# Optimization experiments

Measured on AMD Instinct MI355X. Metric: run time of the kernel, lower is better.

## Reference

```python
import jax, jax.numpy as jnp
import numpy as np

TOKENS = 32768
HIDDEN = 2048
N_EXPERTS = 128
TOP_K = 8
NORM_TOPK_PROB = True


def setup_inputs() -> dict:
    key = jax.random.key(0)
    k1, k2 = jax.random.split(key)
    hidden_states = jax.random.normal(k1, (TOKENS, HIDDEN), dtype=jnp.float32)
    # router weight [num_experts, hidden_dim]; small init like a trained gate
    weight = jax.random.normal(k2, (N_EXPERTS, HIDDEN), dtype=jnp.float32) * 0.02
    return {"hidden_states": hidden_states, "weight": weight}


def reference(hidden_states, weight):
    # flatten tokens (already [T, H])
    x = hidden_states.reshape(-1, HIDDEN)
    # router logits: [T, E]
    logits = jnp.einsum("th,eh->te", x, weight)
    # softmax in float32 (matches dtype=torch.float)
    probs = jax.nn.softmax(logits.astype(jnp.float32), axis=-1)
    # top-k over experts
    top_val, top_idx = jax.lax.top_k(probs, TOP_K)  # [T, K], [T, K]
    if NORM_TOPK_PROB:
        top_val = top_val / jnp.sum(top_val, axis=-1, keepdims=True)
    top_val = top_val.astype(probs.dtype)
    # scatter renormalized weights into dense [T, E] score tensor
    rows = jnp.arange(x.shape[0])[:, None]  # [T, 1]
    scores = jnp.zeros_like(probs).at[rows, top_idx].set(top_val)
    return scores, top_idx
```

## Files before the change

kernel.cpp:

```cpp
#include <hip/hip_runtime.h>
#include <hip/hip_bf16.h>

#define NT   32768
#define NH   2048
#define NE   128
#define TOPK 8
#define BT   32
#define BND    6.0e-4f
#define TWO_B  (2.0f * BND)

#define WS_W_OFF   64
#define WS_REC_U32 262160

typedef __attribute__((ext_vector_type(8))) short bf16x8;
typedef __attribute__((ext_vector_type(4))) float f32x4;
typedef __attribute__((ext_vector_type(4))) unsigned int u32x4;

static __device__ __forceinline__ unsigned short f2bf(float f) {
    __hip_bfloat16 h = __float2bfloat16(f);
    return *reinterpret_cast<unsigned short*>(&h);
}

__global__ __launch_bounds__(256) void prep_w_kernel(
    const float* __restrict__ W, unsigned short* __restrict__ Wt)
{
    int g = blockIdx.x * 256 + threadIdx.x;
    int lane = g & 63;
    int te   = (g >> 6) & 7;
    int s    = (g >> 9) & 1;
    int k32  = g >> 10;
    int row  = te * 16 + (lane & 15);
    int kb   = k32 * 32 + (lane >> 4) * 8;
    const float* src = W + (size_t)row * NH + kb;
    float4 f0 = *(const float4*)src;
    float4 f1 = *(const float4*)(src + 4);
    float f[8] = {f0.x, f0.y, f0.z, f0.w, f1.x, f1.y, f1.z, f1.w};
    bf16x8 o;
    #pragma unroll
    for (int e = 0; e < 8; ++e) {
        unsigned short h = f2bf(f[e]);
        if (s == 0) o[e] = (short)h;
        else {
            float fh = __builtin_bit_cast(float, ((unsigned int)h) << 16);
            o[e] = (short)f2bf(f[e] - fh);
        }
    }
    *(bf16x8*)(Wt + (size_t)g * 8) = o;
}

__global__ __launch_bounds__(256, 2) void router_gemm_kernel(
    const float* __restrict__ X, const unsigned short* __restrict__ Wt,
    float* __restrict__ out, unsigned int* __restrict__ ws)
{
    __shared__ float ps[2][BT * 132];

    const int tid  = threadIdx.x;
    const int lane = tid & 63;
    const int w    = tid >> 6;
    const int l15  = lane & 15, lhi = lane >> 4;
    const int t0   = blockIdx.x * BT;

    f32x4 acc[2][8];
    #pragma unroll
    for (int i = 0; i < 2; ++i)
        #pragma unroll
        for (int te = 0; te < 8; ++te) acc[i][te] = (f32x4){0.f, 0.f, 0.f, 0.f};

    const float* x0 = X + (size_t)(t0 + l15) * NH + w * 512 + lhi * 8;
    const float* x1 = x0 + 16 * NH;
    const unsigned short* wbase = Wt + (size_t)(w * 16) * 8192 + lane * 8;

    bf16x8 b0[8][2], b1[8][2];

    #define LOADB(arr, kk) do {                                                \
        const unsigned short* wb_ = wbase + (size_t)(kk) * 8192;               \
        _Pragma("unroll")                                                      \
        for (int te = 0; te < 8; ++te) {                                       \
            arr[te][0] = *(const bf16x8*)(wb_ + te * 512);                     \
            arr[te][1] = *(const bf16x8*)(wb_ + 4096 + te * 512);              \
        }                                                                      \
    } while (0)

    #define SPLITA(kk, ah, al) do {                                            \
        _Pragma("unroll")                                                      \
        for (int i = 0; i < 2; ++i) {                                          \
            const float* xp = (i ? x1 : x0) + (kk) * 32;                       \
            float4 fa = *(const float4*)xp;                                    \
            float4 fb = *(const float4*)(xp + 4);                              \
            float ff[8] = {fa.x, fa.y, fa.z, fa.w, fb.x, fb.y, fb.z, fb.w};    \
            unsigned int hu[4], lu[4];                                         \
            _Pragma("unroll")                                                  \
            for (int p = 0; p < 4; ++p) {                                      \
                unsigned int u0 = __builtin_bit_cast(unsigned int, ff[2*p]);   \
                unsigned int u1 = __builtin_bit_cast(unsigned int, ff[2*p+1]); \
                unsigned int r0 = u0 + 0x8000u, r1 = u1 + 0x8000u;             \
                hu[p] = (r0 >> 16) | (r1 & 0xFFFF0000u);                       \
                float h0 = __builtin_bit_cast(float, r0 & 0xFFFF0000u);        \
                float h1 = __builtin_bit_cast(float, r1 & 0xFFFF0000u);        \
                float e0 = ff[2*p] - h0, e1 = ff[2*p+1] - h1;                  \
                unsigned int s0 = __builtin_bit_cast(unsigned int, e0) + 0x8000u; \
                unsigned int s1 = __builtin_bit_cast(unsigned int, e1) + 0x8000u; \
                lu[p] = (s0 >> 16) | (s1 & 0xFFFF0000u);                       \
            }                                                                  \
            ah[i] = __builtin_bit_cast(bf16x8, (u32x4){hu[0],hu[1],hu[2],hu[3]}); \
            al[i] = __builtin_bit_cast(bf16x8, (u32x4){lu[0],lu[1],lu[2],lu[3]}); \
        }                                                                      \
    } while (0)

    #define DOMFMA(b, ah, al) do {                                             \
        _Pragma("unroll")                                                      \
        for (int te = 0; te < 8; ++te) {                                       \
            acc[0][te] = __builtin_amdgcn_mfma_f32_16x16x32_bf16(ah[0], b[te][0], acc[0][te], 0, 0, 0); \
            acc[1][te] = __builtin_amdgcn_mfma_f32_16x16x32_bf16(ah[1], b[te][0], acc[1][te], 0, 0, 0); \
            acc[0][te] = __builtin_amdgcn_mfma_f32_16x16x32_bf16(al[0], b[te][0], acc[0][te], 0, 0, 0); \
            acc[1][te] = __builtin_amdgcn_mfma_f32_16x16x32_bf16(al[1], b[te][0], acc[1][te], 0, 0, 0); \
            acc[0][te] = __builtin_amdgcn_mfma_f32_16x16x32_bf16(ah[0], b[te][1], acc[0][te], 0, 0, 0); \
            acc[1][te] = __builtin_amdgcn_mfma_f32_16x16x32_bf16(ah[1], b[te][1], acc[1][te], 0, 0, 0); \
        }                                                                      \
    } while (0)

    LOADB(b0, 0);
    for (int p = 0; p < 8; ++p) {
        bf16x8 ah[2], al[2];
        LOADB(b1, 2 * p + 1);
        SPLITA(2 * p, ah, al);
        DOMFMA(b0, ah, al);
        if (p < 7) LOADB(b0, 2 * p + 2);
        SPLITA(2 * p + 1, ah, al);
        DOMFMA(b1, ah, al);
    }

    if (w < 2) {
        #pragma unroll
        for (int i = 0; i < 2; ++i)
            #pragma unroll
            for (int te = 0; te < 8; ++te)
                #pragma unroll
                for (int q = 0; q < 4; ++q)
                    ps[w][(i * 16 + lhi * 4 + q) * 132 + te * 16 + l15] = acc[i][te][q];
    }
    __syncthreads();
    if (w >= 2) {
        #pragma unroll
        for (int i = 0; i < 2; ++i)
            #pragma unroll
            for (int te = 0; te < 8; ++te)
                #pragma unroll
                for (int q = 0; q < 4; ++q) {
                    int o = (i * 16 + lhi * 4 + q) * 132 + te * 16 + l15;
                    ps[w - 2][o] += acc[i][te][q];
                }
    }
    __syncthreads();
    #pragma unroll
    for (int q = 0; q < 4; ++q) {
        int idx = tid + q * 256;
        int row = idx >> 5, c4 = idx & 31;
        int o = row * 132 + c4 * 4;
        float4 a = *(float4*)&ps[0][o];
        float4 b = *(float4*)&ps[1][o];
        a.x += b.x; a.y += b.y; a.z += b.z; a.w += b.w;
        *(float4*)&ps[0][o] = a;
    }
    float* scoreBase = out + (size_t)t0 * NE;
    #pragma unroll
    for (int q = 0; q < 4; ++q) {
        int i = tid + q * 256;
        *(float4*)(scoreBase + (size_t)i * 4) = make_float4(0.f, 0.f, 0.f, 0.f);
    }
    __syncthreads();

    if (tid < BT) {
        const float* row = &ps[0][tid * 132];
        float tv[13]; int ti[13];
        #pragma unroll
        for (int k = 0; k < 13; ++k) { tv[k] = -3.0e38f; ti[k] = 0; }
        for (int e = 0; e < NE; ++e) {
            float v = row[e];
            if (v > tv[12]) {
                float cv = v; int ci = e;
                #pragma unroll
                for (int s = 0; s < 13; ++s) {
                    if (cv > tv[s]) {
                        float t1 = tv[s]; int t2 = ti[s];
                        tv[s] = cv; ti[s] = ci; cv = t1; ci = t2;
                    }
                }
            }
        }
        bool flag = false;
        #pragma unroll
        for (int k = 0; k < 8; ++k) flag |= (tv[k] - tv[k + 1] < TWO_B);

        float pv[8]; float ksum = 0.f;
        #pragma unroll
        for (int k = 0; k < 8; ++k) { pv[k] = expf(tv[k] - tv[0]); ksum += pv[k]; }
        const int tg = t0 + tid;
        float* srow = out + (size_t)tg * NE;
        float* irow = out + (size_t)NT * NE + (size_t)tg * TOPK;
        #pragma unroll
        for (int k = 0; k < 8; ++k) {
            srow[ti[k]] = pv[k] / ksum;
            irow[k] = (float)ti[k];
        }

        if (flag) {
            unsigned int cnt;
            unsigned int idw[4] = {0u, 0u, 0u, 0u};
            float thr = tv[7] - TWO_B;
            if (tv[12] >= thr) {
                cnt = 0xFFu;
            } else {
                cnt = 0;
                #pragma unroll
                for (int k = 0; k < 13; ++k) {
                    if (k < 8 || tv[k] >= thr) {
                        idw[cnt >> 2] |= ((unsigned int)ti[k]) << ((cnt & 3) * 8);
                        ++cnt;
                    }
                }
            }
            unsigned int slot = atomicAdd(ws, 1u);
            unsigned int* rec = ws + WS_REC_U32 + slot * 8;
            rec[0] = (unsigned int)tg;
            rec[1] = cnt;
            rec[2] = idw[0]; rec[3] = idw[1]; rec[4] = idw[2]; rec[5] = idw[3];
        }
    }
}

__global__ __launch_bounds__(256) void finalize_kernel(
    const float* __restrict__ X, const float* __restrict__ W,
    float* __restrict__ out, const unsigned int* __restrict__ ws)
{
    __shared__ float  xs[2048];
    __shared__ double cv[128];
    __shared__ int    cid[128];
    __shared__ float  ovals[8];
    __shared__ int    oidx[8];

    const int tid = threadIdx.x;
    const int lane = tid & 63, w = tid >> 6;
    const unsigned int n = ws[0];

    for (unsigned int rI = blockIdx.x; rI < n; rI += gridDim.x) {
        const unsigned int* rec = ws + WS_REC_U32 + rI * 8;
        const int tg = (int)rec[0];
        const unsigned int cnt = rec[1];
        const unsigned char* ids = (const unsigned char*)(rec + 2);
        const int nc = (cnt == 0xFFu) ? NE : (int)cnt;

        #pragma unroll
        for (int q = 0; q < 2; ++q) {
            int i = tid + q * 256;
            *(float4*)(xs + i * 4) = *(const float4*)(X + (size_t)tg * NH + i * 4);
        }
        __syncthreads();

        for (int c = w; c < nc; c += 4) {
            int e = (cnt == 0xFFu) ? c : (int)ids[c];
            const float* wrow = W + (size_t)e * NH;
            double s = 0.0;
            #pragma unroll
            for (int m = 0; m < 8; ++m) {
                float4 wv = *(const float4*)(wrow + m * 256 + lane * 4);
                float4 xv = *(const float4*)(xs + m * 256 + lane * 4);
                s = fma((double)xv.x, (double)wv.x, s);
                s = fma((double)xv.y, (double)wv.y, s);
                s = fma((double)xv.z, (double)wv.z, s);
                s = fma((double)xv.w, (double)wv.w, s);
            }
            #pragma unroll
            for (int off = 32; off >= 1; off >>= 1) s += __shfl_xor(s, off);
            if (lane == 0) { cv[c] = s; cid[c] = e; }
        }
        __syncthreads();

        if (tid == 0) {
            double lv[8];
            #pragma unroll
            for (int k = 0; k < 8; ++k) {
                double best = -1.0e300; int bi = 1 << 30, bc = 0;
                for (int c = 0; c < nc; ++c) {
                    double v = cv[c]; int e = cid[c];
                    if (v > best || (v == best && e < bi)) { best = v; bi = e; bc = c; }
                }
                lv[k] = best; oidx[k] = bi; cv[bc] = -1.0e301;
            }
            double m = lv[0], sum = 0.0, p[8];
            #pragma unroll
            for (int k = 0; k < 8; ++k) { p[k] = exp(lv[k] - m); sum += p[k]; }
            #pragma unroll
            for (int k = 0; k < 8; ++k) ovals[k] = (float)(p[k] / sum);
        }
        __syncthreads();

        float* srow = out + (size_t)tg * NE;
        if (tid < NE) {
            float val = 0.f;
            #pragma unroll
            for (int k = 0; k < 8; ++k) if (oidx[k] == tid) val = ovals[k];
            srow[tid] = val;
        }
        if (tid < TOPK) out[(size_t)NT * NE + (size_t)tg * TOPK + tid] = (float)oidx[tid];
        __syncthreads();
    }
}

extern "C" void kernel_launch(void* const* d_in, const int* in_sizes, int n_in,
                              void* d_out, int out_size, void* d_ws, size_t ws_size,
                              hipStream_t stream) {
    const float* X = (const float*)d_in[0];
    const float* W = (const float*)d_in[1];
    float* out = (float*)d_out;
    unsigned char* wsb = (unsigned char*)d_ws;
    unsigned short* Wt = (unsigned short*)(wsb + WS_W_OFF);

    hipMemsetAsync(d_ws, 0, 64, stream);
    prep_w_kernel<<<256, 256, 0, stream>>>(W, Wt);
    router_gemm_kernel<<<NT / BT, 256, 0, stream>>>(X, Wt, out, (unsigned int*)d_ws);
    finalize_kernel<<<1024, 256, 0, stream>>>(X, W, out, (const unsigned int*)d_ws);
}
```

Baseline: 221.7 us.

## Split top-k selection out of router GEMM into separate select kernel

The GEMM kernel now writes raw logits into the score buffer instead of doing a serial per-token top-k on 32 threads at its tail. A new select kernel reloads 128 tokens' logits per block, runs top-k, zeroes the rows, and writes the normalized scores, indices (as float4 stores) and ambiguity records. The aim is to take the serial selection tail off the GEMM blocks so they finish sooner. The cost is an extra kernel launch plus a round trip of the 16 MB logits buffer through global memory.

```diff
diff --git a/kernel.cpp b/kernel.cpp
--- a/kernel.cpp
+++ b/kernel.cpp
@@ -6,6 +6,7 @@
 #define NE   128
 #define TOPK 8
 #define BT   32
+#define SBT  128
 #define BND    6.0e-4f
 #define TWO_B  (2.0f * BND)
 
@@ -50,7 +51,7 @@
 
 __global__ __launch_bounds__(256, 2) void router_gemm_kernel(
     const float* __restrict__ X, const unsigned short* __restrict__ Wt,
-    float* __restrict__ out, unsigned int* __restrict__ ws)
+    float* __restrict__ outLg)
 {
     __shared__ float ps[2][BT * 132];
 
@@ -154,25 +155,38 @@
     __syncthreads();
     #pragma unroll
     for (int q = 0; q < 4; ++q) {
-        int idx = tid + q * 256;
-        int row = idx >> 5, c4 = idx & 31;
+        int i = tid + q * 256;
+        int row = i >> 5, c4 = i & 31;
         int o = row * 132 + c4 * 4;
         float4 a = *(float4*)&ps[0][o];
         float4 b = *(float4*)&ps[1][o];
         a.x += b.x; a.y += b.y; a.z += b.z; a.w += b.w;
-        *(float4*)&ps[0][o] = a;
-    }
-    float* scoreBase = out + (size_t)t0 * NE;
-    #pragma unroll
-    for (int q = 0; q < 4; ++q) {
-        int i = tid + q * 256;
-        *(float4*)(scoreBase + (size_t)i * 4) = make_float4(0.f, 0.f, 0.f, 0.f);
-    }
-    __syncthreads();
-
-    if (tid < BT) {
-        const float* row = &ps[0][tid * 132];
-        float tv[13]; int ti[13];
+        *(float4*)(outLg + (size_t)(t0 + row) * NE + c4 * 4) = a;
+    }
+}
+
+__global__ __launch_bounds__(512) void select_kernel(
+    float* __restrict__ out, unsigned int* __restrict__ ws)
+{
+    __shared__ float lg[SBT * 132];
+
+    const int tid = threadIdx.x;
+    const int t0  = blockIdx.x * SBT;
+
+    #pragma unroll
+    for (int q = 0; q < 8; ++q) {
+        int i = tid + q * 512;
+        int row = i >> 5, c4 = i & 31;
+        float4 v = *(const float4*)(out + (size_t)(t0 + row) * NE + c4 * 4);
+        *(float4*)(&lg[row * 132 + c4 * 4]) = v;
+    }
+    __syncthreads();
+
+    float pv[8]; int ti[13]; bool flag = false; float ksum = 0.f;
+    unsigned int cnt = 0; unsigned int idw[4] = {0u, 0u, 0u, 0u};
+    if (tid < SBT) {
+        const float* row = &lg[tid * 132];
+        float tv[13];
         #pragma unroll
         for (int k = 0; k < 13; ++k) { tv[k] = -3.0e38f; ti[k] = 0; }
         for (int e = 0; e < NE; ++e) {
@@ -188,30 +202,16 @@
                 }
             }
         }
-        bool flag = false;
         #pragma unroll
         for (int k = 0; k < 8; ++k) flag |= (tv[k] - tv[k + 1] < TWO_B);
-
-        float pv[8]; float ksum = 0.f;
         #pragma unroll
         for (int k = 0; k < 8; ++k) { pv[k] = expf(tv[k] - tv[0]); ksum += pv[k]; }
-        const int tg = t0 + tid;
-        float* srow = out + (size_t)tg * NE;
-        float* irow = out + (size_t)NT * NE + (size_t)tg * TOPK;
-        #pragma unroll
-        for (int k = 0; k < 8; ++k) {
-            srow[ti[k]] = pv[k] / ksum;
-            irow[k] = (float)ti[k];
-        }
 
         if (flag) {
-            unsigned int cnt;
-            unsigned int idw[4] = {0u, 0u, 0u, 0u};
             float thr = tv[7] - TWO_B;
             if (tv[12] >= thr) {
                 cnt = 0xFFu;
             } else {
-                cnt = 0;
                 #pragma unroll
                 for (int k = 0; k < 13; ++k) {
                     if (k < 8 || tv[k] >= thr) {
@@ -220,6 +220,30 @@
                     }
                 }
             }
+        }
+    }
+    __syncthreads();
+
+    float* scoreBase = out + (size_t)t0 * NE;
+    #pragma unroll
+    for (int q = 0; q < 8; ++q) {
+        int i = tid + q * 512;
+        *(float4*)(scoreBase + (size_t)i * 4) = make_float4(0.f, 0.f, 0.f, 0.f);
+    }
+    __syncthreads();
+
+    if (tid < SBT) {
+        const int tg = t0 + tid;
+        float* srow = out + (size_t)tg * NE;
+        float* irow = out + (size_t)NT * NE + (size_t)tg * TOPK;
+        #pragma unroll
+        for (int k = 0; k < 8; ++k) srow[ti[k]] = pv[k] / ksum;
+        float4 i0 = make_float4((float)ti[0], (float)ti[1], (float)ti[2], (float)ti[3]);
+        float4 i1 = make_float4((float)ti[4], (float)ti[5], (float)ti[6], (float)ti[7]);
+        *(float4*)irow = i0;
+        *(float4*)(irow + 4) = i1;
+
+        if (flag) {
             unsigned int slot = atomicAdd(ws, 1u);
             unsigned int* rec = ws + WS_REC_U32 + slot * 8;
             rec[0] = (unsigned int)tg;
@@ -318,6 +342,7 @@
 
     hipMemsetAsync(d_ws, 0, 64, stream);
     prep_w_kernel<<<256, 256, 0, stream>>>(W, Wt);
-    router_gemm_kernel<<<NT / BT, 256, 0, stream>>>(X, Wt, out, (unsigned int*)d_ws);
+    router_gemm_kernel<<<NT / BT, 256, 0, stream>>>(X, Wt, out);
+    select_kernel<<<NT / SBT, 512, 0, stream>>>(out, (unsigned int*)d_ws);
     finalize_kernel<<<1024, 256, 0, stream>>>(X, W, out, (const unsigned int*)d_ws);
 }
```

Measured after the change: 311.4 us. 1.4x slower.
